# Kernel optimization log

Hardware: AMD Instinct MI355X
Metric: run time of the kernel (lower is better)

## Reference

```python
import jax, jax.numpy as jnp
import numpy as np


def setup_inputs() -> dict:
    key = jax.random.key(0)
    k1, k2, k3 = jax.random.split(key, 3)
    N, M, D = 8192, 8192, 64
    return {
        "query": jax.random.normal(k1, (N, D), dtype=jnp.float32),
        "key": jax.random.normal(k2, (M, D), dtype=jnp.float32),
        "value": jax.random.normal(k3, (M, D), dtype=jnp.float32),
        "hyper_c": 1,
        "num_of_method": 2,
    }


def reference(query, key, value, hyper_c, num_of_method):
    # num_of_method == 2 (default): cosine-similarity scores scaled by hyper_c.
    # L2-normalize rows (dim=1), matmul, scale, softmax over keys, weight values.
    q_norm = query / jnp.linalg.norm(query, axis=1, keepdims=True)
    k_norm = key / jnp.linalg.norm(key, axis=1, keepdims=True)
    scores = hyper_c * jnp.einsum("nd,md->nm", q_norm, k_norm)  # [N, M]
    p_attn = jax.nn.softmax(scores, axis=-1)
    res_query = jnp.einsum("nm,md->nd", p_attn, value)  # [N, D]
    return (res_query, p_attn)
```

## Files before the change

kernel.cpp:

```cpp
#include <hip/hip_runtime.h>
#include <hip/hip_bf16.h>
#include <cstdint>
#include <cstddef>

#define NQ 8192
#define NK 8192
#define DD 64
#define KSPLIT 4
#define KRANGE (NK / KSPLIT)
#define KTILE 128
#define NT (KRANGE / KTILE)

typedef __bf16 bf16x8 __attribute__((ext_vector_type(8)));
typedef float f32x16 __attribute__((ext_vector_type(16)));
typedef unsigned short u16;
typedef uint32_t u32;

static __device__ __forceinline__ u16 f2bf(float f) {
    union { float f; uint32_t u; } v; v.f = f;
    uint32_t r = (v.u + 0x7fffu + ((v.u >> 16) & 1u)) >> 16;
    return (u16)r;
}

static __device__ __forceinline__ u32 cvtpk(float lo, float hi) {
    u32 r;
    asm("v_cvt_pk_bf16_f32 %0, %1, %2" : "=v"(r) : "v"(lo), "v"(hi));
    return r;
}

#define GLOAD16(g, l)                                                          \
    __builtin_amdgcn_global_load_lds(                                          \
        (__attribute__((address_space(1))) void*)(g),                          \
        (__attribute__((address_space(3))) void*)(l), 16, 0, 0)

__global__ void k_norm(const float* __restrict__ q, const float* __restrict__ k,
                       u16* __restrict__ qn, u16* __restrict__ kn) {
    int wid  = (blockIdx.x * blockDim.x + threadIdx.x) >> 6;
    int lane = threadIdx.x & 63;
    int nw   = (gridDim.x * blockDim.x) >> 6;
    for (int row = wid; row < 2 * NQ; row += nw) {
        const float* src = (row < NQ) ? q : k;
        u16* dst = (row < NQ) ? qn : kn;
        int r = row & (NQ - 1);
        float x = src[(size_t)r * DD + lane];
        float ss = x * x;
        #pragma unroll
        for (int m = 1; m < 64; m <<= 1) ss += __shfl_xor(ss, m, 64);
        dst[(size_t)r * DD + lane] = f2bf(x * rsqrtf(ss));
    }
}

__global__ void k_transv(const float* __restrict__ v, u16* __restrict__ vT) {
    __shared__ float ts[64][65];
    int mb = blockIdx.x * 64;
    int t = threadIdx.x;
    #pragma unroll
    for (int i = 0; i < 16; i++) {
        int idx = i * 256 + t;
        int r = idx >> 6, c = idx & 63;
        ts[r][c] = v[(size_t)(mb + r) * DD + c];
    }
    __syncthreads();
    #pragma unroll
    for (int i = 0; i < 16; i++) {
        int idx = i * 256 + t;
        int d = idx >> 6, m = idx & 63;
        vT[(size_t)d * NK + mb + m] = f2bf(ts[m][d]);
    }
}

__global__ __launch_bounds__(256, 2) void
k_flash(const u16* __restrict__ qn, const u16* __restrict__ kn,
        const u16* __restrict__ vT, const int* __restrict__ hcp,
        float* __restrict__ prs, float* __restrict__ ppv) {
    __shared__ __align__(16) u16 qs[32 * 64];
    __shared__ __align__(16) union SmT {
        struct { u16 ks[128 * 64]; u16 vs[64 * 128]; } t[2];
        struct { float redA[32 * 64]; float redB[32 * 64]; } ep;
    } sm;
    __shared__ float rs_ws[4][32];

    const float hc = (float)hcp[0];
    const int t = threadIdx.x;
    const int w = t >> 6;
    const int lane = t & 63;
    const int l31 = lane & 31;
    const int half = lane >> 5;
    const int qb = (blockIdx.x >> 2) * 32;
    const int sp = blockIdx.x & 3;
    const int k0 = sp * KRANGE;
    const int kw = w * 32;

#define STAGE_KV(B, KB)                                                        \
    do {                                                                       \
        const u16* ksrc_ = kn + (size_t)(k0 + (KB) * KTILE) * DD;              \
        const u16* vsrc_ = vT + (size_t)(k0 + (KB) * KTILE);                   \
        _Pragma("unroll")                                                      \
        for (int i_ = 0; i_ < 4; i_++) {                                       \
            int idx_ = (w * 4 + i_) * 64 + lane;                               \
            int kr_ = idx_ >> 3, kc_ = idx_ & 7;                               \
            GLOAD16(ksrc_ + (size_t)kr_ * DD + ((kc_ ^ (kr_ & 7)) * 8),        \
                    &sm.t[B].ks[(w * 4 + i_) * 512]);                          \
            int vr_ = idx_ >> 4, vc_ = idx_ & 15;                              \
            GLOAD16(vsrc_ + (size_t)vr_ * NK + ((vc_ ^ (vr_ & 7)) * 8),        \
                    &sm.t[B].vs[(w * 4 + i_) * 512]);                          \
        }                                                                      \
    } while (0)

    {
        int row = t >> 3, c = t & 7;
        *reinterpret_cast<uint4*>(&qs[row * 64 + ((c ^ (row & 7)) * 8)]) =
            *reinterpret_cast<const uint4*>(&qn[(size_t)(qb + row) * DD + c * 8]);
    }

    float rs_sum = 0.f;
    f32x16 pv0, pv1;
    #pragma unroll
    for (int i = 0; i < 16; i++) { pv0[i] = 0.f; pv1[i] = 0.f; }

    STAGE_KV(0, 0);
    __syncthreads();

    int cur = 0;
    for (int kb = 0; kb < NT; kb++) {
        if (kb + 1 < NT) STAGE_KV(cur ^ 1, kb + 1);

        const u16* ks_ = sm.t[cur].ks;
        const u16* vs_ = sm.t[cur].vs;

        f32x16 acc;
        #pragma unroll
        for (int i = 0; i < 16; i++) acc[i] = 0.f;
        #pragma unroll
        for (int s = 0; s < 4; s++) {
            int ca = 2 * s + half;
            int kr = kw + l31;
            bf16x8 af = *reinterpret_cast<const bf16x8*>(&ks_[kr * 64 + ((ca ^ (kr & 7)) * 8)]);
            bf16x8 bf = *reinterpret_cast<const bf16x8*>(&qs[l31 * 64 + ((ca ^ (l31 & 7)) * 8)]);
            acc = __builtin_amdgcn_mfma_f32_32x32x16_bf16(af, bf, acc, 0, 0, 0);
        }
        float e[16];
        #pragma unroll
        for (int r = 0; r < 16; r++) {
            e[r] = __expf(acc[r] * hc);
            rs_sum += e[r];
        }
        bf16x8 pa[2];
        #pragma unroll
        for (int s = 0; s < 2; s++) {
            u32 x0 = cvtpk(e[8 * s + 0], e[8 * s + 1]);
            u32 y0 = cvtpk(e[8 * s + 4], e[8 * s + 5]);
            auto r0 = __builtin_amdgcn_permlane32_swap(x0, y0, false, false);
            u32 x1 = cvtpk(e[8 * s + 2], e[8 * s + 3]);
            u32 y1 = cvtpk(e[8 * s + 6], e[8 * s + 7]);
            auto r1 = __builtin_amdgcn_permlane32_swap(x1, y1, false, false);
            union { u32 u[4]; bf16x8 v; } f;
            f.u[0] = r0[0]; f.u[1] = r1[0]; f.u[2] = r0[1]; f.u[3] = r1[1];
            pa[s] = f.v;
        }
        #pragma unroll
        for (int s = 0; s < 2; s++) {
            int cv = (kw >> 3) + 2 * s + half;
            int vr0 = l31, vr1 = 32 + l31;
            bf16x8 b0 = *reinterpret_cast<const bf16x8*>(&vs_[vr0 * 128 + ((cv ^ (vr0 & 7)) * 8)]);
            bf16x8 b1 = *reinterpret_cast<const bf16x8*>(&vs_[vr1 * 128 + ((cv ^ (vr1 & 7)) * 8)]);
            pv0 = __builtin_amdgcn_mfma_f32_32x32x16_bf16(pa[s], b0, pv0, 0, 0, 0);
            pv1 = __builtin_amdgcn_mfma_f32_32x32x16_bf16(pa[s], b1, pv1, 0, 0, 0);
        }

        __syncthreads();
        cur ^= 1;
    }

    rs_sum += __shfl_xor(rs_sum, 32, 64);
    if (lane < 32) rs_ws[w][lane] = rs_sum;
    __syncthreads();
    if (t < 32)
        prs[(size_t)sp * NQ + qb + t] =
            rs_ws[0][t] + rs_ws[1][t] + rs_ws[2][t] + rs_ws[3][t];

    float* redA = sm.ep.redA;
    float* redB = sm.ep.redB;
    if (w == 0) {
        #pragma unroll
        for (int r = 0; r < 16; r++) {
            int qq = (r & 3) + 8 * (r >> 2) + 4 * half;
            redA[qq * 64 + l31] = pv0[r];
            redA[qq * 64 + 32 + l31] = pv1[r];
        }
    } else if (w == 1) {
        #pragma unroll
        for (int r = 0; r < 16; r++) {
            int qq = (r & 3) + 8 * (r >> 2) + 4 * half;
            redB[qq * 64 + l31] = pv0[r];
            redB[qq * 64 + 32 + l31] = pv1[r];
        }
    }
    __syncthreads();
    if (w == 2) {
        #pragma unroll
        for (int r = 0; r < 16; r++) {
            int qq = (r & 3) + 8 * (r >> 2) + 4 * half;
            redA[qq * 64 + l31] += pv0[r];
            redA[qq * 64 + 32 + l31] += pv1[r];
        }
    } else if (w == 3) {
        #pragma unroll
        for (int r = 0; r < 16; r++) {
            int qq = (r & 3) + 8 * (r >> 2) + 4 * half;
            redB[qq * 64 + l31] += pv0[r];
            redB[qq * 64 + 32 + l31] += pv1[r];
        }
    }
    __syncthreads();
    float* dst = ppv + (size_t)sp * NQ * DD + (size_t)qb * DD;
    #pragma unroll
    for (int i = 0; i < 8; i++) {
        int idx = i * 256 + t;
        dst[idx] = redA[idx] + redB[idx];
    }
#undef STAGE_KV
}

__global__ void k_reduce(const float* __restrict__ prs, const float* __restrict__ ppv,
                         float* __restrict__ inv_rs, float* __restrict__ out_res) {
    int id = blockIdx.x * blockDim.x + threadIdx.x;
    int n = id >> 6, d = id & 63;
    float s = prs[n] + prs[NQ + n] + prs[2 * NQ + n] + prs[3 * NQ + n];
    float inv = 1.0f / s;
    if (d == 0) inv_rs[n] = inv;
    const size_t st = (size_t)NQ * DD;
    float v = ppv[id] + ppv[st + id] + ppv[2 * st + id] + ppv[3 * st + id];
    out_res[id] = v * inv;
}

__global__ __launch_bounds__(256, 4) void
k_pwrite(const u16* __restrict__ qn, const u16* __restrict__ kn,
         const float* __restrict__ inv_rs, const int* __restrict__ hcp,
         float* __restrict__ out_p) {
    __shared__ __align__(16) u16 qs2[64 * 64];
    __shared__ __align__(16) u16 ks2[64 * 64];
    __shared__ float invl[64];

    const float hc = (float)hcp[0];
    const int bid = blockIdx.x;
    const int qb = (bid >> 7) * 64;
    const int kb = (bid & 127) * 64;
    const int t = threadIdx.x;
    const int w = t >> 6;
    const int lane = t & 63;
    const int l31 = lane & 31;
    const int half = lane >> 5;

    #pragma unroll
    for (int i = 0; i < 2; i++) {
        int idx16 = (w * 2 + i) * 64 + lane;
        int row = idx16 >> 3, c = idx16 & 7;
        GLOAD16(qn + (size_t)(qb + row) * DD + ((c ^ (row & 7)) * 8),
                &qs2[(w * 2 + i) * 512]);
        GLOAD16(kn + (size_t)(kb + row) * DD + ((c ^ (row & 7)) * 8),
                &ks2[(w * 2 + i) * 512]);
    }
    if (t < 64) invl[t] = inv_rs[qb + t];
    __syncthreads();

    const int wq = (w >> 1) * 32, wk = (w & 1) * 32;
    f32x16 acc;
    #pragma unroll
    for (int i = 0; i < 16; i++) acc[i] = 0.f;
    #pragma unroll
    for (int s = 0; s < 4; s++) {
        int ca = 2 * s + half;
        int qr = wq + l31, kr = wk + l31;
        bf16x8 a = *reinterpret_cast<const bf16x8*>(&qs2[qr * 64 + ((ca ^ (qr & 7)) * 8)]);
        bf16x8 b = *reinterpret_cast<const bf16x8*>(&ks2[kr * 64 + ((ca ^ (kr & 7)) * 8)]);
        acc = __builtin_amdgcn_mfma_f32_32x32x16_bf16(a, b, acc, 0, 0, 0);
    }
    #pragma unroll
    for (int r = 0; r < 16; r++) {
        int qq = wq + (r & 3) + 8 * (r >> 2) + 4 * half;
        out_p[(size_t)(qb + qq) * NK + kb + wk + l31] = __expf(acc[r] * hc) * invl[qq];
    }
}

extern "C" void kernel_launch(void* const* d_in, const int* in_sizes, int n_in,
                              void* d_out, int out_size, void* d_ws, size_t ws_size,
                              hipStream_t stream) {
    const float* q = (const float*)d_in[0];
    const float* k = (const float*)d_in[1];
    const float* v = (const float*)d_in[2];
    const int* hc = (const int*)d_in[3];

    float* out_res = (float*)d_out;
    float* out_p = out_res + (size_t)NQ * DD;

    char* wsb = (char*)d_ws;
    u16* qn = (u16*)wsb;
    u16* kn = qn + (size_t)NQ * DD;
    u16* vT = kn + (size_t)NK * DD;
    float* inv_rs = (float*)(vT + (size_t)NK * DD);

    const size_t base_need = 3 * (size_t)NQ * DD * 2 + (size_t)NQ * 4;
    const size_t extra_need = (size_t)KSPLIT * NQ * 4 + (size_t)KSPLIT * NQ * DD * 4;
    char* extra = (ws_size >= base_need + extra_need)
                      ? wsb + base_need
                      : (char*)out_p + ((size_t)NQ * NK * 4 - extra_need);
    float* prs = (float*)extra;
    float* ppv = prs + (size_t)KSPLIT * NQ;

    k_norm<<<1024, 256, 0, stream>>>(q, k, qn, kn);
    k_transv<<<NK / 64, 256, 0, stream>>>(v, vT);
    k_flash<<<(NQ / 32) * KSPLIT, 256, 0, stream>>>(qn, kn, vT, hc, prs, ppv);
    k_reduce<<<(NQ * DD) / 256, 256, 0, stream>>>(prs, ppv, inv_rs, out_res);
    k_pwrite<<<(NQ / 64) * (NK / 64), 256, 0, stream>>>(qn, kn, inv_rs, hc, out_p);
}
```

Measured before the change: 334.8 us.

## Loop k_pwrite over eight key tiles with double-buffered K and vectorized stores

The probability-write kernel now has each block reuse one query tile across eight key tiles, double-buffering the key tiles in shared memory so the next load overlaps the current MFMA. It swaps the MFMA operands so the accumulator layout puts four consecutive key columns in each lane, which allows float4 stores instead of scalar stores to the large 256MB output. The goal is better store coalescing and fewer redundant Q loads, at the cost of 8x fewer blocks and a barrier per tile.

```diff
diff --git a/kernel.cpp b/kernel.cpp
--- a/kernel.cpp
+++ b/kernel.cpp
@@ -239,18 +239,18 @@
          const float* __restrict__ inv_rs, const int* __restrict__ hcp,
          float* __restrict__ out_p) {
     __shared__ __align__(16) u16 qs2[64 * 64];
-    __shared__ __align__(16) u16 ks2[64 * 64];
-    __shared__ float invl[64];
+    __shared__ __align__(16) u16 ks2[2][64 * 64];
 
     const float hc = (float)hcp[0];
     const int bid = blockIdx.x;
-    const int qb = (bid >> 7) * 64;
-    const int kb = (bid & 127) * 64;
+    const int qb = (bid >> 4) * 64;
+    const int kt0 = (bid & 15) * 8;
     const int t = threadIdx.x;
     const int w = t >> 6;
     const int lane = t & 63;
     const int l31 = lane & 31;
     const int half = lane >> 5;
+    const int wq = (w >> 1) * 32, wk = (w & 1) * 32;
 
     #pragma unroll
     for (int i = 0; i < 2; i++) {
@@ -258,29 +258,54 @@
         int row = idx16 >> 3, c = idx16 & 7;
         GLOAD16(qn + (size_t)(qb + row) * DD + ((c ^ (row & 7)) * 8),
                 &qs2[(w * 2 + i) * 512]);
-        GLOAD16(kn + (size_t)(kb + row) * DD + ((c ^ (row & 7)) * 8),
-                &ks2[(w * 2 + i) * 512]);
-    }
-    if (t < 64) invl[t] = inv_rs[qb + t];
-    __syncthreads();
-
-    const int wq = (w >> 1) * 32, wk = (w & 1) * 32;
-    f32x16 acc;
-    #pragma unroll
-    for (int i = 0; i < 16; i++) acc[i] = 0.f;
-    #pragma unroll
-    for (int s = 0; s < 4; s++) {
-        int ca = 2 * s + half;
-        int qr = wq + l31, kr = wk + l31;
-        bf16x8 a = *reinterpret_cast<const bf16x8*>(&qs2[qr * 64 + ((ca ^ (qr & 7)) * 8)]);
-        bf16x8 b = *reinterpret_cast<const bf16x8*>(&ks2[kr * 64 + ((ca ^ (kr & 7)) * 8)]);
-        acc = __builtin_amdgcn_mfma_f32_32x32x16_bf16(a, b, acc, 0, 0, 0);
-    }
-    #pragma unroll
-    for (int r = 0; r < 16; r++) {
-        int qq = wq + (r & 3) + 8 * (r >> 2) + 4 * half;
-        out_p[(size_t)(qb + qq) * NK + kb + wk + l31] = __expf(acc[r] * hc) * invl[qq];
-    }
+    }
+#define STAGE_K(B, KT)                                                         \
+    do {                                                                       \
+        const u16* ksrc_ = kn + (size_t)(KT) * 64 * DD;                        \
+        _Pragma("unroll")                                                      \
+        for (int i_ = 0; i_ < 2; i_++) {                                       \
+            int idx_ = (w * 2 + i_) * 64 + lane;                               \
+            int row_ = idx_ >> 3, c_ = idx_ & 7;                               \
+            GLOAD16(ksrc_ + (size_t)row_ * DD + ((c_ ^ (row_ & 7)) * 8),       \
+                    &ks2[B][(w * 2 + i_) * 512]);                              \
+        }                                                                      \
+    } while (0)
+
+    STAGE_K(0, kt0);
+    const float iv = inv_rs[qb + wq + l31];
+    float* rowp = out_p + (size_t)(qb + wq + l31) * NK;
+    const int qr = wq + l31;
+    __syncthreads();
+
+    int cur = 0;
+    for (int i = 0; i < 8; i++) {
+        if (i + 1 < 8) STAGE_K(cur ^ 1, kt0 + i + 1);
+
+        f32x16 acc;
+        #pragma unroll
+        for (int j = 0; j < 16; j++) acc[j] = 0.f;
+        #pragma unroll
+        for (int s = 0; s < 4; s++) {
+            int ca = 2 * s + half;
+            int kr = wk + l31;
+            bf16x8 a = *reinterpret_cast<const bf16x8*>(&ks2[cur][kr * 64 + ((ca ^ (kr & 7)) * 8)]);
+            bf16x8 b = *reinterpret_cast<const bf16x8*>(&qs2[qr * 64 + ((ca ^ (qr & 7)) * 8)]);
+            acc = __builtin_amdgcn_mfma_f32_32x32x16_bf16(a, b, acc, 0, 0, 0);
+        }
+        const int colb = (kt0 + i) * 64 + wk + 4 * half;
+        #pragma unroll
+        for (int g = 0; g < 4; g++) {
+            float4 vv;
+            vv.x = __expf(acc[4 * g + 0] * hc) * iv;
+            vv.y = __expf(acc[4 * g + 1] * hc) * iv;
+            vv.z = __expf(acc[4 * g + 2] * hc) * iv;
+            vv.w = __expf(acc[4 * g + 3] * hc) * iv;
+            *reinterpret_cast<float4*>(rowp + colb + 8 * g) = vv;
+        }
+        __syncthreads();
+        cur ^= 1;
+    }
+#undef STAGE_K
 }
 
 extern "C" void kernel_launch(void* const* d_in, const int* in_sizes, int n_in,
@@ -312,5 +337,5 @@
     k_transv<<<NK / 64, 256, 0, stream>>>(v, vT);
     k_flash<<<(NQ / 32) * KSPLIT, 256, 0, stream>>>(qn, kn, vT, hc, prs, ppv);
     k_reduce<<<(NQ * DD) / 256, 256, 0, stream>>>(prs, ppv, inv_rs, out_res);
-    k_pwrite<<<(NQ / 64) * (NK / 64), 256, 0, stream>>>(qn, kn, inv_rs, hc, out_p);
-}
+    k_pwrite<<<(NQ / 64) * (NK / 64) / 8, 256, 0, stream>>>(qn, kn, inv_rs, hc, out_p);
+}
```

New measurement: 377.4 us. 12.7% more time.
